# Kernel optimization log

Measured on AMD Instinct MI355X. Metric: run time of the kernel, lower is better.

Reference implementation:

```python
import jax, jax.numpy as jnp
import numpy as np

D_MODEL = 512
NUM_HEADS = 8
D_HEAD = D_MODEL // NUM_HEADS
QMAX = 127.0  # int8 narrow-range symmetric
EPS = 1e-8


def _quant_dequant_weight(w):
    # per-output-channel symmetric int8 quant-dequant (brevitas default style)
    s = jnp.maximum(jnp.max(jnp.abs(w), axis=1, keepdims=True) / QMAX, EPS)
    return jnp.clip(jnp.round(w / s), -QMAX, QMAX) * s


def _quant_dequant_act(x):
    # per-tensor symmetric int8 quant-dequant (QuantIdentity)
    s = jnp.maximum(jnp.max(jnp.abs(x)) / QMAX, EPS)
    return jnp.clip(jnp.round(x / s), -QMAX, QMAX) * s


def _qlinear(x, w, b):
    return jnp.einsum('btd,od->bto', x, _quant_dequant_weight(w)) + b


def setup_inputs() -> dict:
    key = jax.random.key(0)
    ks = jax.random.split(key, 10)
    B, T = 2, 4096
    lim = 1.0 / np.sqrt(D_MODEL)
    mk = lambda k: jax.random.uniform(k, (D_MODEL, D_MODEL), jnp.float32, -lim, lim)
    mb = lambda k: jax.random.uniform(k, (D_MODEL,), jnp.float32, -lim, lim)
    return {
        'x': jax.random.normal(ks[0], (B, T, D_MODEL), jnp.float32),
        'mask': jax.random.randint(ks[1], (B, T), 0, 2, jnp.int32),
        'Wq': mk(ks[2]), 'bq': mb(ks[3]),
        'Wk': mk(ks[4]), 'bk': mb(ks[5]),
        'Wv': mk(ks[6]), 'bv': mb(ks[7]),
        'Wo': mk(ks[8]), 'bo': mb(ks[9]),
    }


def reference(x, mask, Wq, bq, Wk, bk, Wv, bv, Wo, bo):
    B, T, _ = x.shape
    shape = lambda t: t.reshape(B, T, NUM_HEADS, D_HEAD).transpose(0, 2, 1, 3)  # (B,H,T,dh)
    q = shape(_qlinear(x, Wq, bq))
    k = shape(_qlinear(x, Wk, bk))
    v = shape(_qlinear(x, Wv, bv))
    scores = jnp.einsum('bhtd,bhsd->bhts', q, k) / np.sqrt(D_HEAD)
    keep = (mask != 0)[:, None, None, :]  # (B,1,1,T), 0 = masked
    scores = jnp.where(keep, scores, -jnp.inf)
    attn = jax.nn.softmax(scores, axis=-1)
    ctx = jnp.einsum('bhts,bhsd->bhtd', attn, v)
    ctx = ctx.transpose(0, 2, 1, 3).reshape(B, T, D_MODEL)
    out = _qlinear(ctx, Wo, bo)
    return _quant_dequant_act(out)
```

## Files before the change

kernel.cpp:

```cpp
#include <hip/hip_runtime.h>
#include <hip/hip_bf16.h>

typedef __bf16 bf16;
typedef __bf16 bf16x8 __attribute__((ext_vector_type(8)));
typedef __bf16 bf16x4v __attribute__((ext_vector_type(4)));
typedef float f32x4 __attribute__((ext_vector_type(4)));

#define D_MODEL 512
#define T_SEQ   4096
#define NH      8
#define DH      64
#define M_ROWS  8192
#define VROW    8224
#define QK_SCALE 0.18033688011112042f

__device__ __forceinline__ void gload16(const void* g, void* l) {
  __builtin_amdgcn_global_load_lds(
      (const __attribute__((address_space(1))) unsigned int*)g,
      (__attribute__((address_space(3))) unsigned int*)l, 16, 0, 0);
}

__global__ __launch_bounds__(64) void detect_dtype(const unsigned short* __restrict__ xr,
                                                   int* __restrict__ flag)
{
  int lane = threadIdx.x;
  int cnt = 0;
  for (int i = lane; i < 4096; i += 64) {
    unsigned short u = xr[i];
    int e = (u >> 7) & 0xFF;
    bool insane = (e >= 133) || (e > 0 && e <= 96) || (e == 0 && (u & 0x7F) != 0);
    cnt += insane ? 1 : 0;
  }
#pragma unroll
  for (int off = 32; off >= 1; off >>= 1) cnt += __shfl_xor(cnt, off);
  if (lane == 0) *flag = (cnt > 400) ? 1 : 0;
}

__global__ __launch_bounds__(256) void convert_x(const void* __restrict__ xr,
                                                 const int* __restrict__ flag,
                                                 bf16* __restrict__ xb, int n)
{
  int i = (blockIdx.x * blockDim.x + threadIdx.x) * 4;
  if (i >= n) return;
  if (*flag) {
    float4 v = *(const float4*)((const float*)xr + i);
    __align__(8) bf16 o[4] = {(bf16)v.x, (bf16)v.y, (bf16)v.z, (bf16)v.w};
    *(uint2*)(xb + i) = *(uint2*)o;
  } else {
    *(uint2*)(xb + i) = *(const uint2*)((const bf16*)xr + i);
  }
}

__global__ __launch_bounds__(1024) void prep_aux(
    const void* b0, const void* b1, const void* b2, const void* b3,
    const int* __restrict__ mask,
    const int* __restrict__ flag, float* __restrict__ bf, float* __restrict__ mf)
{
  const void* ps[4] = {b0, b1, b2, b3};
  int fl = *flag;
  for (int t = threadIdx.x; t < 4 * D_MODEL; t += 1024) {
    int w = t >> 9, o = t & 511;
    bf[t] = fl ? ((const float*)ps[w])[o] : (float)((const bf16*)ps[w])[o];
  }
  for (int j = threadIdx.x; j < M_ROWS; j += 1024)
    mf[j] = mask[j] ? -16.0f : -1e30f;
}

__global__ __launch_bounds__(256) void qdq_weights(
    const void* __restrict__ Wq, const void* __restrict__ Wk,
    const void* __restrict__ Wv, const void* __restrict__ Wo,
    const int* __restrict__ flag, bf16* __restrict__ out)
{
  int wave = threadIdx.x >> 6, lane = threadIdx.x & 63;
  int gid = blockIdx.x * 4 + wave;
  int w = gid >> 9, row = gid & 511;
  const void* W = (w == 0) ? Wq : (w == 1) ? Wk : (w == 2) ? Wv : Wo;
  int fl = *flag;
  float v[8]; float amax = 0.f;
#pragma unroll
  for (int i = 0; i < 8; i++) {
    int idx = row * D_MODEL + lane + 64 * i;
    v[i] = fl ? ((const float*)W)[idx] : (float)((const bf16*)W)[idx];
    amax = fmaxf(amax, fabsf(v[i]));
  }
#pragma unroll
  for (int off = 32; off >= 1; off >>= 1) amax = fmaxf(amax, __shfl_xor(amax, off));
  float s = fmaxf(amax / 127.0f, 1e-8f);
  bf16* dst = out + (size_t)gid * D_MODEL;
#pragma unroll
  for (int i = 0; i < 8; i++) {
    float q = rintf(v[i] / s);
    q = fminf(fmaxf(q, -127.f), 127.f);
    dst[lane + 64*i] = (bf16)(q * s);
  }
}

#define LDS_STRIDE 40
__global__ __launch_bounds__(256) void gemm_qkv(
    const bf16* __restrict__ A, const bf16* __restrict__ W,
    const float* __restrict__ bias,
    bf16* __restrict__ Qh, bf16* __restrict__ Kh, bf16* __restrict__ VTP)
{
  __shared__ __align__(16) bf16 As[128 * LDS_STRIDE];
  __shared__ __align__(16) bf16 Bs[128 * LDS_STRIDE];

  const int tid = threadIdx.x;
  const int wave = tid >> 6, lane = tid & 63;
  const int lr = lane & 15, quad = lane >> 4;
  const int wm = (wave >> 1) * 64, wn = (wave & 1) * 64;
  const int m0 = blockIdx.x * 128, n0 = blockIdx.y * 128;
  const int sec = blockIdx.y >> 2;

  f32x4 acc[4][4];
#pragma unroll
  for (int i = 0; i < 4; i++)
#pragma unroll
    for (int j = 0; j < 4; j++) acc[i][j] = f32x4{0.f, 0.f, 0.f, 0.f};

  const int srow = tid >> 2;
  const int sseg = (tid & 3) * 8;

  for (int k0 = 0; k0 < D_MODEL; k0 += 32) {
#pragma unroll
    for (int i = 0; i < 2; i++) {
      int r = srow + i * 64;
      *(uint4*)&As[r * LDS_STRIDE + sseg] = *(const uint4*)(A + (size_t)(m0 + r) * D_MODEL + k0 + sseg);
      *(uint4*)&Bs[r * LDS_STRIDE + sseg] = *(const uint4*)(W + (size_t)(n0 + r) * D_MODEL + k0 + sseg);
    }
    __syncthreads();
    bf16x8 af[4], bfr[4];
#pragma unroll
    for (int mt = 0; mt < 4; mt++) af[mt]  = *(bf16x8*)&As[(wm + mt*16 + lr) * LDS_STRIDE + quad*8];
#pragma unroll
    for (int nt = 0; nt < 4; nt++) bfr[nt] = *(bf16x8*)&Bs[(wn + nt*16 + lr) * LDS_STRIDE + quad*8];
#pragma unroll
    for (int mt = 0; mt < 4; mt++)
#pragma unroll
      for (int nt = 0; nt < 4; nt++)
        acc[mt][nt] = __builtin_amdgcn_mfma_f32_16x16x32_bf16(af[mt], bfr[nt], acc[mt][nt], 0, 0, 0);
    __syncthreads();
  }

  const float scale = (sec == 0) ? QK_SCALE : 1.0f;
#pragma unroll
  for (int mt = 0; mt < 4; mt++) {
    int grow = m0 + wm + mt * 16 + quad * 4;
#pragma unroll
    for (int nt = 0; nt < 4; nt++) {
      int gcol = n0 + wn + nt * 16 + lr;
      float b = bias[gcol];
      if (sec == 2) {
        bf16x4v pk;
#pragma unroll
        for (int r = 0; r < 4; r++) pk[r] = (bf16)(acc[mt][nt][r] + b);
        *(bf16x4v*)(VTP + (size_t)(gcol - 1024) * VROW + grow) = pk;
      } else {
        bf16* dst = (sec == 0) ? Qh : Kh;
        int c = gcol & 511;
        int hh = c >> 6, c64 = c & 63;
#pragma unroll
        for (int r = 0; r < 4; r++) {
          int row = grow + r;
          int bb = row >> 12, t = row & 4095;
          dst[((size_t)(bb * NH + hh) * T_SEQ + t) * DH + c64] =
              (bf16)((acc[mt][nt][r] + b) * scale);
        }
      }
    }
  }
}

__global__ __launch_bounds__(256) void gemm_o(
    const bf16* __restrict__ A, const bf16* __restrict__ W,
    const float* __restrict__ bias,
    float* __restrict__ Cf, unsigned int* __restrict__ amaxp)
{
  __shared__ __align__(16) bf16 As[64 * LDS_STRIDE];
  __shared__ __align__(16) bf16 Bs[128 * LDS_STRIDE];
  __shared__ float wred[4];

  const int tid = threadIdx.x;
  const int wave = tid >> 6, lane = tid & 63;
  const int lr = lane & 15, quad = lane >> 4;
  const int wm = (wave >> 1) * 32, wn = (wave & 1) * 64;
  const int m0 = blockIdx.x * 64, n0 = blockIdx.y * 128;

  f32x4 acc[2][4];
#pragma unroll
  for (int i = 0; i < 2; i++)
#pragma unroll
    for (int j = 0; j < 4; j++) acc[i][j] = f32x4{0.f, 0.f, 0.f, 0.f};

  const int srow = tid >> 2;
  const int sseg = (tid & 3) * 8;

  for (int k0 = 0; k0 < D_MODEL; k0 += 32) {
    *(uint4*)&As[srow * LDS_STRIDE + sseg] = *(const uint4*)(A + (size_t)(m0 + srow) * D_MODEL + k0 + sseg);
#pragma unroll
    for (int i = 0; i < 2; i++) {
      int r = srow + i * 64;
      *(uint4*)&Bs[r * LDS_STRIDE + sseg] = *(const uint4*)(W + (size_t)(n0 + r) * D_MODEL + k0 + sseg);
    }
    __syncthreads();
    bf16x8 af[2], bfr[4];
#pragma unroll
    for (int mt = 0; mt < 2; mt++) af[mt]  = *(bf16x8*)&As[(wm + mt*16 + lr) * LDS_STRIDE + quad*8];
#pragma unroll
    for (int nt = 0; nt < 4; nt++) bfr[nt] = *(bf16x8*)&Bs[(wn + nt*16 + lr) * LDS_STRIDE + quad*8];
#pragma unroll
    for (int mt = 0; mt < 2; mt++)
#pragma unroll
      for (int nt = 0; nt < 4; nt++)
        acc[mt][nt] = __builtin_amdgcn_mfma_f32_16x16x32_bf16(af[mt], bfr[nt], acc[mt][nt], 0, 0, 0);
    __syncthreads();
  }

  float lmax = 0.f;
#pragma unroll
  for (int mt = 0; mt < 2; mt++) {
    int grow = m0 + wm + mt * 16 + quad * 4;
#pragma unroll
    for (int nt = 0; nt < 4; nt++) {
      int gcol = n0 + wn + nt * 16 + lr;
      float b = bias[gcol];
#pragma unroll
      for (int r = 0; r < 4; r++) {
        float v = acc[mt][nt][r] + b;
        Cf[(size_t)(grow + r) * D_MODEL + gcol] = v;
        lmax = fmaxf(lmax, fabsf(v));
      }
    }
  }
#pragma unroll
  for (int off = 32; off >= 1; off >>= 1) lmax = fmaxf(lmax, __shfl_xor(lmax, off));
  if (lane == 0) wred[wave] = lmax;
  __syncthreads();
  if (tid == 0) {
    float m = fmaxf(fmaxf(wred[0], wred[1]), fmaxf(wred[2], wred[3]));
    atomicMax(amaxp, __float_as_uint(m));
  }
}

__global__ __launch_bounds__(256, 2) void attn(
    const bf16* __restrict__ Q, const bf16* __restrict__ K, const bf16* __restrict__ VT,
    const float* __restrict__ maskf, bf16* __restrict__ ctx)
{
  __shared__ __align__(16) bf16 Ks[2][64 * 64];
  __shared__ __align__(16) bf16 Vs[2][64 * 64];
  __shared__ __align__(16) float Mf[T_SEQ];

  const int tid = threadIdx.x;
  const int wave = tid >> 6, lane = tid & 63;
  const int lr = lane & 15, quad = lane >> 4;
  const int i = blockIdx.x;
  const int bh = (i & 7) * 2 + ((i >> 3) & 1);
  const int qb = i >> 4;
  const int b = bh >> 3, h = bh & 7;
  const int q0 = qb * 128 + wave * 32;

  const bf16* Qb = Q + (size_t)bh * T_SEQ * DH;
  const bf16* Kb = K + (size_t)bh * T_SEQ * DH;
  const bf16* Vb = VT + (size_t)(h * DH) * VROW + (size_t)b * T_SEQ;
  const float* mb = maskf + b * T_SEQ;

  const int phase = (qb * 2) & 63;
  int cc = phase;

  const bf16* kSrc[2]; const bf16* vSrc[2];
#pragma unroll
  for (int ii = 0; ii < 2; ii++) {
    int s = ii * 256 + tid, row = s >> 3, sl = s & 7;
    int kt = row >> 4, m = row & 15;
    int keym = ((m >> 2) << 3) + ((kt & 1) << 2) + (m & 3) + ((kt >> 1) << 5);
    kSrc[ii] = Kb + (size_t)keym * DH + ((sl ^ (row & 7)) << 3);
    vSrc[ii] = Vb + (size_t)row * VROW + ((sl ^ (row & 7)) << 3);
  }

#pragma unroll
  for (int ii = 0; ii < 4; ii++) {
    int g = ii * 256 + tid;
    gload16(mb + g * 4, &Mf[g * 4]);
  }
  {
    int kb = cc * 64;
#pragma unroll
    for (int ii = 0; ii < 2; ii++) {
      int s = ii * 256 + tid;
      gload16(kSrc[ii] + (size_t)kb * DH, &Ks[0][s * 8]);
      gload16(vSrc[ii] + kb, &Vs[0][s * 8]);
    }
  }

  bf16x8 qf[2][2];
#pragma unroll
  for (int qt = 0; qt < 2; qt++) {
    const bf16* rq = Qb + (size_t)(q0 + qt * 16 + lr) * DH;
    qf[qt][0] = *(const bf16x8*)(rq + quad * 8);
    qf[qt][1] = *(const bf16x8*)(rq + 32 + quad * 8);
  }

  f32x4 O[2][4];
#pragma unroll
  for (int a = 0; a < 2; a++)
#pragma unroll
    for (int c = 0; c < 4; c++) O[a][c] = f32x4{0.f, 0.f, 0.f, 0.f};
  float lacc[2] = {0.f, 0.f};

  __syncthreads();

  int cur = 0;
  for (int j = 0; j < 64; j++) {
    const bool nxt = (j + 1) < 64;
    const int ccn = (cc + 1) & 63;

    if (nxt) {
      int kb = ccn * 64;
#pragma unroll
      for (int ii = 0; ii < 2; ii++) {
        int s = ii * 256 + tid;
        gload16(kSrc[ii] + (size_t)kb * DH, &Ks[cur ^ 1][s * 8]);
        gload16(vSrc[ii] + kb, &Vs[cur ^ 1][s * 8]);
      }
    }

    f32x4 mk[4];
#pragma unroll
    for (int kt = 0; kt < 4; kt++)
      mk[kt] = *(const f32x4*)&Mf[cc * 64 + ((kt >> 1) << 5) + (quad << 3) + ((kt & 1) << 2)];

    bf16x8 kr[4][2];
#pragma unroll
    for (int kt = 0; kt < 4; kt++)
#pragma unroll
      for (int kh = 0; kh < 2; kh++)
        kr[kt][kh] = *(const bf16x8*)&Ks[cur][(kt * 16 + lr) * 64 +
                                             (((kh * 4 + quad) ^ (lr & 7)) << 3)];

    bf16x8 pfa[2][2];
#pragma unroll
    for (int qt = 0; qt < 2; qt++) {
      f32x4 z[4];
#pragma unroll
      for (int kt = 0; kt < 4; kt++) {
        f32x4 t = mk[kt];
        t = __builtin_amdgcn_mfma_f32_16x16x32_bf16(kr[kt][0], qf[qt][0], t, 0, 0, 0);
        t = __builtin_amdgcn_mfma_f32_16x16x32_bf16(kr[kt][1], qf[qt][1], t, 0, 0, 0);
        z[kt] = t;
      }
      float la = lacc[qt];
#pragma unroll
      for (int kt = 0; kt < 4; kt++) {
#pragma unroll
        for (int r = 0; r < 4; r++) {
          float p = __builtin_amdgcn_exp2f(z[kt][r]);
          la += p;
          pfa[qt][kt >> 1][((kt & 1) << 2) + r] = (bf16)p;
        }
      }
      lacc[qt] = la;
    }

    bf16x8 vr[4][2];
#pragma unroll
    for (int nt = 0; nt < 4; nt++)
#pragma unroll
      for (int ks = 0; ks < 2; ks++)
        vr[nt][ks] = *(const bf16x8*)&Vs[cur][(nt * 16 + lr) * 64 +
                                             (((ks * 4 + quad) ^ (lr & 7)) << 3)];

#pragma unroll
    for (int nt = 0; nt < 4; nt++)
#pragma unroll
      for (int qt = 0; qt < 2; qt++) {
        O[qt][nt] = __builtin_amdgcn_mfma_f32_16x16x32_bf16(pfa[qt][0], vr[nt][0], O[qt][nt], 0, 0, 0);
        O[qt][nt] = __builtin_amdgcn_mfma_f32_16x16x32_bf16(pfa[qt][1], vr[nt][1], O[qt][nt], 0, 0, 0);
      }

    __syncthreads();
    cur ^= 1; cc = ccn;
  }

#pragma unroll
  for (int qt = 0; qt < 2; qt++) {
    float ls = lacc[qt];
    ls += __shfl_xor(ls, 16);
    ls += __shfl_xor(ls, 32);
    float linv = 1.0f / ls;
    float lO[4];
#pragma unroll
    for (int r = 0; r < 4; r++) lO[r] = __shfl(linv, quad * 4 + r);
#pragma unroll
    for (int nt = 0; nt < 4; nt++)
#pragma unroll
      for (int r = 0; r < 4; r++) {
        size_t row = (size_t)(b * T_SEQ + q0 + qt * 16 + quad * 4 + r);
        ctx[row * D_MODEL + h * DH + nt * 16 + lr] = (bf16)(O[qt][nt][r] * lO[r]);
      }
  }
}

__global__ __launch_bounds__(256) void act_qdq(
    const float* __restrict__ pre, const unsigned int* __restrict__ amaxp,
    const int* __restrict__ flag, void* __restrict__ outv, int n)
{
  int i = (blockIdx.x * blockDim.x + threadIdx.x) * 4;
  if (i >= n) return;
  float s = fmaxf(__uint_as_float(*amaxp) / 127.0f, 1e-8f);
  float4 v = *(const float4*)(pre + i);
  float o[4] = {v.x, v.y, v.z, v.w};
#pragma unroll
  for (int r = 0; r < 4; r++) {
    float q = rintf(o[r] / s);
    q = fminf(fmaxf(q, -127.f), 127.f);
    o[r] = q * s;
  }
  if (*flag) {
    *(float4*)((float*)outv + i) = make_float4(o[0], o[1], o[2], o[3]);
  } else {
    __align__(8) bf16 ob[4] = {(bf16)o[0], (bf16)o[1], (bf16)o[2], (bf16)o[3]};
    *(uint2*)((bf16*)outv + i) = *(uint2*)ob;
  }
}

extern "C" void kernel_launch(void* const* d_in, const int* in_sizes, int n_in,
                              void* d_out, int out_size, void* d_ws, size_t ws_size,
                              hipStream_t stream) {
  const void* x    = d_in[0];
  const int*  mask = (const int*)d_in[1];
  const void* Wq = d_in[2]; const void* bq = d_in[3];
  const void* Wk = d_in[4]; const void* bk = d_in[5];
  const void* Wv = d_in[6]; const void* bv = d_in[7];
  const void* Wo = d_in[8]; const void* bo = d_in[9];

  char* ws = (char*)d_ws;
  int*  flag  = (int*)(ws + 0);
  unsigned int* amax = (unsigned int*)(ws + 64);
  float* biasf = (float*)(ws + 1024);
  float* maskf = (float*)(ws + 16384);
  bf16* Wt  = (bf16*)(ws + 65536);
  bf16* xb  = (bf16*)(ws + 4194304);
  bf16* Qm  = (bf16*)(ws + 12582912);
  bf16* Km  = (bf16*)(ws + 20971520);
  bf16* VT  = (bf16*)(ws + 29360128);
  bf16* Cm  = (bf16*)(ws + 4194304);
  float* pre = (float*)(ws + 12582912);

  hipMemsetAsync(amax, 0, 4, stream);
  detect_dtype<<<1, 64, 0, stream>>>((const unsigned short*)x, flag);
  convert_x<<<4096, 256, 0, stream>>>(x, flag, xb, M_ROWS * D_MODEL);
  prep_aux<<<1, 1024, 0, stream>>>(bq, bk, bv, bo, mask, flag, biasf, maskf);
  qdq_weights<<<512, 256, 0, stream>>>(Wq, Wk, Wv, Wo, flag, Wt);
  gemm_qkv<<<dim3(64, 12), 256, 0, stream>>>(xb, Wt, biasf, Qm, Km, VT);
  attn<<<512, 256, 0, stream>>>(Qm, Km, VT, maskf, Cm);
  gemm_o<<<dim3(128, 4), 256, 0, stream>>>(Cm, Wt + 3*262144, biasf + 1536, pre, amax);
  act_qdq<<<4096, 256, 0, stream>>>(pre, amax, flag, d_out, M_ROWS * D_MODEL);
}
```

Measured before the change: 223.8 us.

## Triple-buffer K/V tiles in attention with explicit vmcnt waits; parallelize prep_aux

The attention kernel moves from double to triple buffering of the K and V LDS tiles. Loads are issued two tiles ahead, and the __syncthreads calls become raw s_barrier plus s_waitcnt vmcnt with partial counts, so global-to-LDS transfers can overlap more compute. LDS use grows by 16KB per block, which may reduce occupancy, and the hand-counted vmcnt values are fragile. Separately, prep_aux now launches 8 blocks instead of a single 1024-thread block looping over the mask.

```diff
diff --git a/kernel.cpp b/kernel.cpp
--- a/kernel.cpp
+++ b/kernel.cpp
@@ -19,6 +19,9 @@
       (const __attribute__((address_space(1))) unsigned int*)g,
       (__attribute__((address_space(3))) unsigned int*)l, 16, 0, 0);
 }
+
+#define WAITV(N) asm volatile("s_waitcnt vmcnt(" #N ")" ::: "memory")
+#define CFENCE   asm volatile("" ::: "memory")
 
 __global__ __launch_bounds__(64) void detect_dtype(const unsigned short* __restrict__ xr,
                                                    int* __restrict__ flag)
@@ -58,12 +61,12 @@
 {
   const void* ps[4] = {b0, b1, b2, b3};
   int fl = *flag;
-  for (int t = threadIdx.x; t < 4 * D_MODEL; t += 1024) {
-    int w = t >> 9, o = t & 511;
-    bf[t] = fl ? ((const float*)ps[w])[o] : (float)((const bf16*)ps[w])[o];
-  }
-  for (int j = threadIdx.x; j < M_ROWS; j += 1024)
-    mf[j] = mask[j] ? -16.0f : -1e30f;
+  int g = blockIdx.x * 1024 + threadIdx.x;
+  if (g < 4 * D_MODEL) {
+    int w = g >> 9, o = g & 511;
+    bf[g] = fl ? ((const float*)ps[w])[o] : (float)((const bf16*)ps[w])[o];
+  }
+  mf[g] = mask[g] ? -16.0f : -1e30f;
 }
 
 __global__ __launch_bounds__(256) void qdq_weights(
@@ -245,8 +248,8 @@
     const bf16* __restrict__ Q, const bf16* __restrict__ K, const bf16* __restrict__ VT,
     const float* __restrict__ maskf, bf16* __restrict__ ctx)
 {
-  __shared__ __align__(16) bf16 Ks[2][64 * 64];
-  __shared__ __align__(16) bf16 Vs[2][64 * 64];
+  __shared__ __align__(16) bf16 Ks[3][64 * 64];
+  __shared__ __align__(16) bf16 Vs[3][64 * 64];
   __shared__ __align__(16) float Mf[T_SEQ];
 
   const int tid = threadIdx.x;
@@ -264,7 +267,6 @@
   const float* mb = maskf + b * T_SEQ;
 
   const int phase = (qb * 2) & 63;
-  int cc = phase;
 
   const bf16* kSrc[2]; const bf16* vSrc[2];
 #pragma unroll
@@ -276,21 +278,6 @@
     vSrc[ii] = Vb + (size_t)row * VROW + ((sl ^ (row & 7)) << 3);
   }
 
-#pragma unroll
-  for (int ii = 0; ii < 4; ii++) {
-    int g = ii * 256 + tid;
-    gload16(mb + g * 4, &Mf[g * 4]);
-  }
-  {
-    int kb = cc * 64;
-#pragma unroll
-    for (int ii = 0; ii < 2; ii++) {
-      int s = ii * 256 + tid;
-      gload16(kSrc[ii] + (size_t)kb * DH, &Ks[0][s * 8]);
-      gload16(vSrc[ii] + kb, &Vs[0][s * 8]);
-    }
-  }
-
   bf16x8 qf[2][2];
 #pragma unroll
   for (int qt = 0; qt < 2; qt++) {
@@ -298,6 +285,23 @@
     qf[qt][0] = *(const bf16x8*)(rq + quad * 8);
     qf[qt][1] = *(const bf16x8*)(rq + 32 + quad * 8);
   }
+  WAITV(0);
+
+#pragma unroll
+  for (int ii = 0; ii < 4; ii++) {
+    int g = ii * 256 + tid;
+    gload16(mb + g * 4, &Mf[g * 4]);
+  }
+#pragma unroll
+  for (int d = 0; d < 3; d++) {
+    int kb = ((phase + d) & 63) * 64;
+#pragma unroll
+    for (int ii = 0; ii < 2; ii++) {
+      int s = ii * 256 + tid;
+      gload16(kSrc[ii] + (size_t)kb * DH, &Ks[d][s * 8]);
+      gload16(vSrc[ii] + kb, &Vs[d][s * 8]);
+    }
+  }
 
   f32x4 O[2][4];
 #pragma unroll
@@ -306,23 +310,12 @@
     for (int c = 0; c < 4; c++) O[a][c] = f32x4{0.f, 0.f, 0.f, 0.f};
   float lacc[2] = {0.f, 0.f};
 
-  __syncthreads();
-
-  int cur = 0;
+  WAITV(8);
+  __builtin_amdgcn_s_barrier();
+  CFENCE;
+
+  int cur = 0, cc = phase;
   for (int j = 0; j < 64; j++) {
-    const bool nxt = (j + 1) < 64;
-    const int ccn = (cc + 1) & 63;
-
-    if (nxt) {
-      int kb = ccn * 64;
-#pragma unroll
-      for (int ii = 0; ii < 2; ii++) {
-        int s = ii * 256 + tid;
-        gload16(kSrc[ii] + (size_t)kb * DH, &Ks[cur ^ 1][s * 8]);
-        gload16(vSrc[ii] + kb, &Vs[cur ^ 1][s * 8]);
-      }
-    }
-
     f32x4 mk[4];
 #pragma unroll
     for (int kt = 0; kt < 4; kt++)
@@ -376,8 +369,28 @@
         O[qt][nt] = __builtin_amdgcn_mfma_f32_16x16x32_bf16(pfa[qt][1], vr[nt][1], O[qt][nt], 0, 0, 0);
       }
 
-    __syncthreads();
-    cur ^= 1; cc = ccn;
+    if (j < 63) {
+      __builtin_amdgcn_s_barrier();
+      CFENCE;
+      if (j < 61) {
+        int kb = ((cc + 3) & 63) * 64;
+#pragma unroll
+        for (int ii = 0; ii < 2; ii++) {
+          int s = ii * 256 + tid;
+          gload16(kSrc[ii] + (size_t)kb * DH, &Ks[cur][s * 8]);
+          gload16(vSrc[ii] + kb, &Vs[cur][s * 8]);
+        }
+        WAITV(8);
+      } else if (j == 61) {
+        WAITV(4);
+      } else {
+        WAITV(0);
+      }
+      __builtin_amdgcn_s_barrier();
+      CFENCE;
+    }
+    cur = (cur == 2) ? 0 : cur + 1;
+    cc = (cc + 1) & 63;
   }
 
 #pragma unroll
@@ -448,7 +461,7 @@
   hipMemsetAsync(amax, 0, 4, stream);
   detect_dtype<<<1, 64, 0, stream>>>((const unsigned short*)x, flag);
   convert_x<<<4096, 256, 0, stream>>>(x, flag, xb, M_ROWS * D_MODEL);
-  prep_aux<<<1, 1024, 0, stream>>>(bq, bk, bv, bo, mask, flag, biasf, maskf);
+  prep_aux<<<8, 1024, 0, stream>>>(bq, bk, bv, bo, mask, flag, biasf, maskf);
   qdq_weights<<<512, 256, 0, stream>>>(Wq, Wk, Wv, Wo, flag, Wt);
   gemm_qkv<<<dim3(64, 12), 256, 0, stream>>>(xb, Wt, biasf, Qm, Km, VT);
   attn<<<512, 256, 0, stream>>>(Qm, Km, VT, maskf, Cm);
```

Result: faster. 216.7 us (-3.2%).
